# Kernel optimization log

Hardware: AMD Instinct MI355X
Metric: run time of the kernel (lower is better)

Reference implementation:

```python
import jax, jax.numpy as jnp
import numpy as np

B, CIN, COUT, H, W = 8, 128, 128, 64, 64
KH = KW = 3
STRIDE = PAD = 1
DIL = 1
K = KH * KW
EPS = 1e-4


def setup_inputs() -> dict:
    key = jax.random.key(0)
    k1, k2, k3 = jax.random.split(key, 3)
    Ho = (H + 2 * PAD - DIL * (KH - 1) - 1) // STRIDE + 1
    Wo = (W + 2 * PAD - DIL * (KW - 1) - 1) // STRIDE + 1
    x = jax.random.normal(k1, (B, CIN, H, W), dtype=jnp.float32)
    offset = jax.random.normal(k2, (B, 2 * K, Ho, Wo), dtype=jnp.float32)
    weight = jax.random.normal(k3, (COUT, CIN, KH, KW), dtype=jnp.float32) * 0.05
    return {"x": x, "offset": offset, "weight": weight}


def _bilinear_gather(x, py, px):
    # x: [B, C, H, W]; py/px: [B, K, Ho, Wo] float sampling positions
    Bn, C, Hn, Wn = x.shape
    x_flat = x.reshape(Bn, C, Hn * Wn)
    y0 = jnp.floor(py)
    x0 = jnp.floor(px)
    ly = py - y0  # fractional parts
    lx = px - x0
    out = 0.0
    corners = [(0.0, 0.0, (1 - ly) * (1 - lx)), (0.0, 1.0, (1 - ly) * lx),
               (1.0, 0.0, ly * (1 - lx)), (1.0, 1.0, ly * lx)]
    for dy, dx, wgt in corners:
        yy = y0 + dy
        xx = x0 + dx
        valid = (yy >= 0) & (yy < Hn) & (xx >= 0) & (xx < Wn)
        yi = jnp.clip(yy, 0, Hn - 1).astype(jnp.int32)
        xi = jnp.clip(xx, 0, Wn - 1).astype(jnp.int32)
        idx = (yi * Wn + xi).reshape(Bn, -1)  # [B, K*Ho*Wo]
        g = jax.vmap(lambda xf, ib: jnp.take(xf, ib, axis=1))(x_flat, idx)  # [B, C, N]
        out = out + g * (wgt * valid.astype(x.dtype)).reshape(Bn, 1, -1)
    return out  # [B, C, K*Ho*Wo]


def reference(x, offset, weight) -> jnp.ndarray:
    Bn = x.shape[0]
    Ho, Wo = offset.shape[2], offset.shape[3]
    # --- weight normalization (per output channel, per kernel tap) ---
    norm_fac = (KH * KW) ** 0.5
    length = jnp.sqrt(jnp.sum(jnp.square(weight) + EPS, axis=1, keepdims=True))  # [O,1,kh,kw]
    wn = weight / length / norm_fac  # [O, Cin, kh, kw]
    # --- sampling positions ---
    off = offset.reshape(Bn, K, 2, Ho, Wo)
    off_y, off_x = off[:, :, 0], off[:, :, 1]
    ky, kx = jnp.meshgrid(jnp.arange(KH), jnp.arange(KW), indexing="ij")
    ky = (ky.reshape(K) * DIL).astype(jnp.float32)
    kx = (kx.reshape(K) * DIL).astype(jnp.float32)
    base_y = (jnp.arange(Ho) * STRIDE - PAD).astype(jnp.float32)
    base_x = (jnp.arange(Wo) * STRIDE - PAD).astype(jnp.float32)
    py = base_y[None, None, :, None] + ky[None, :, None, None] + off_y  # [B,K,Ho,Wo]
    px = base_x[None, None, None, :] + kx[None, :, None, None] + off_x
    # --- deformable im2col + GEMM ---
    cols = _bilinear_gather(x, py, px).reshape(Bn, CIN, K, Ho, Wo)
    out = jnp.einsum("bckhw,ock->bohw", cols, wn.reshape(COUT, CIN, K))
    return out
```

## Files before the change

### kernel.cpp

```cpp
#include <hip/hip_runtime.h>
#include <math.h>


typedef __attribute__((ext_vector_type(8))) short short8;
typedef __attribute__((ext_vector_type(4))) float floatx4;

static __device__ __forceinline__ unsigned int f2bf(float f) {
    unsigned int u = __float_as_uint(f);
    u += 0x7fffu + ((u >> 16) & 1u);
    return u >> 16;
}
static __device__ __forceinline__ float bflo(unsigned int w) {
    return __uint_as_float(w << 16);
}
static __device__ __forceinline__ float bfhi(unsigned int w) {
    return __uint_as_float(w & 0xffff0000u);
}

__global__ void wnorm_k(const float* __restrict__ w, unsigned short* __restrict__ wb) {
    const int ok = blockIdx.x;
    const int o = ok / 9, k = ok % 9;
    const int lane = threadIdx.x;
    const float v0 = w[o * 1152 + lane * 9 + k];
    const float v1 = w[o * 1152 + (lane + 64) * 9 + k];
    float s = v0 * v0 + v1 * v1;
    #pragma unroll
    for (int d = 32; d >= 1; d >>= 1) s += __shfl_xor(s, d, 64);
    const float inv = 1.0f / (3.0f * sqrtf(s + 0.0128f));
    wb[((k * 16 + (lane >> 3)) * 128 + o) * 8 + (lane & 7)]     = (unsigned short)f2bf(v0 * inv);
    wb[((k * 16 + 8 + (lane >> 3)) * 128 + o) * 8 + (lane & 7)] = (unsigned short)f2bf(v1 * inv);
}

__global__ void xpose_k(const float* __restrict__ x, unsigned int* __restrict__ xt32) {
    __shared__ float lds[128 * 65];
    const int b = blockIdx.x >> 6, h = blockIdx.x & 63;
    const int tid = threadIdx.x;
    const float* xp = x + (b * 128 * 64 + h) * 64;
    #pragma unroll 4
    for (int i = 0; i < 32; i++) {
        const int c = i * 4 + (tid >> 6);
        const int ww = tid & 63;
        lds[c * 65 + ww] = xp[c * 4096 + ww];
    }
    __syncthreads();
    unsigned int* xo = xt32 + blockIdx.x * 4096;
    #pragma unroll 4
    for (int i = 0; i < 16; i++) {
        const int flat2 = i * 256 + tid;
        const int ww = flat2 >> 6, cp = flat2 & 63;
        const unsigned int lo = f2bf(lds[(2 * cp) * 65 + ww]);
        const unsigned int hi = f2bf(lds[(2 * cp + 1) * 65 + ww]);
        xo[flat2] = lo | (hi << 16);
    }
}

__global__ __launch_bounds__(256, 2) void dconv_k(
    const unsigned short* __restrict__ xt, const float* __restrict__ off,
    const unsigned short* __restrict__ wb, float* __restrict__ out)
{
    __shared__ float4 tapw[576];
    __shared__ int4   tapi[576];
    __shared__ alignas(16) unsigned short colsS[16 * 520];
    __shared__ alignas(16) unsigned short wS[16 * 128 * 8];

    const int bh = blockIdx.x, b = bh >> 6, ho = bh & 63;
    const int tid = threadIdx.x;

    for (int t = tid; t < 576; t += 256) {
        const int k = t >> 6, p = t & 63;
        const int oidx = ((b * 18 + 2 * k) * 64 + ho) * 64 + p;
        const float offy = off[oidx];
        const float offx = off[oidx + 4096];
        const float py = (float)(ho - 1 + (k / 3)) + offy;
        const float px = (float)(p - 1 + (k % 3)) + offx;
        const float y0f = floorf(py), x0f = floorf(px);
        const float ly = py - y0f, lx = px - x0f;
        const int y0 = (int)y0f, x0 = (int)x0f;
        const int y1 = y0 + 1, x1 = x0 + 1;
        const float vy0 = (y0 >= 0 && y0 < 64) ? 1.0f : 0.0f;
        const float vy1 = (y1 >= 0 && y1 < 64) ? 1.0f : 0.0f;
        const float vx0 = (x0 >= 0 && x0 < 64) ? 1.0f : 0.0f;
        const float vx1 = (x1 >= 0 && x1 < 64) ? 1.0f : 0.0f;
        const int yc0 = min(max(y0, 0), 63), yc1 = min(max(y1, 0), 63);
        const int xc0 = min(max(x0, 0), 63), xc1 = min(max(x1, 0), 63);
        tapw[t] = make_float4((1.0f - ly) * (1.0f - lx) * vy0 * vx0,
                              (1.0f - ly) * lx          * vy0 * vx1,
                              ly * (1.0f - lx)          * vy1 * vx0,
                              ly * lx                   * vy1 * vx1);
        tapi[t] = make_int4((yc0 * 64 + xc0) * 128, (yc0 * 64 + xc1) * 128,
                            (yc1 * 64 + xc0) * 128, (yc1 * 64 + xc1) * 128);
    }
    __syncthreads();

    const int lane = tid & 63, wv = tid >> 6;
    const int quad = lane >> 4, l16 = lane & 15;
    const int g = tid & 15, prow = tid >> 4;
    const unsigned short* xb = xt + b * (64 * 64 * 128);
    const int wbase = wv * 32;

    floatx4 acc0[4], acc1[4];
    #pragma unroll
    for (int t = 0; t < 4; t++) {
        acc0[t] = (floatx4)0.0f;
        acc1[t] = (floatx4)0.0f;
    }

    for (int k = 0; k < 9; k++) {
        const uint4* wsrc = (const uint4*)(wb + k * 16384);
        uint4* wdst = (uint4*)wS;
        #pragma unroll
        for (int i = 0; i < 8; i++) wdst[i * 256 + tid] = wsrc[i * 256 + tid];

        #pragma unroll
        for (int i = 0; i < 4; i++) {
            const int p = i * 16 + prow;
            const float4 wvv = tapw[k * 64 + p];
            const int4  iv  = tapi[k * 64 + p];
            const uint4 r0 = *(const uint4*)(xb + iv.x + g * 8);
            const uint4 r1 = *(const uint4*)(xb + iv.y + g * 8);
            const uint4 r2 = *(const uint4*)(xb + iv.z + g * 8);
            const uint4 r3 = *(const uint4*)(xb + iv.w + g * 8);
            uint4 pk;
            {
                const float lo = wvv.x*bflo(r0.x) + wvv.y*bflo(r1.x) + wvv.z*bflo(r2.x) + wvv.w*bflo(r3.x);
                const float hi = wvv.x*bfhi(r0.x) + wvv.y*bfhi(r1.x) + wvv.z*bfhi(r2.x) + wvv.w*bfhi(r3.x);
                pk.x = f2bf(lo) | (f2bf(hi) << 16);
            }
            {
                const float lo = wvv.x*bflo(r0.y) + wvv.y*bflo(r1.y) + wvv.z*bflo(r2.y) + wvv.w*bflo(r3.y);
                const float hi = wvv.x*bfhi(r0.y) + wvv.y*bfhi(r1.y) + wvv.z*bfhi(r2.y) + wvv.w*bfhi(r3.y);
                pk.y = f2bf(lo) | (f2bf(hi) << 16);
            }
            {
                const float lo = wvv.x*bflo(r0.z) + wvv.y*bflo(r1.z) + wvv.z*bflo(r2.z) + wvv.w*bflo(r3.z);
                const float hi = wvv.x*bfhi(r0.z) + wvv.y*bfhi(r1.z) + wvv.z*bfhi(r2.z) + wvv.w*bfhi(r3.z);
                pk.z = f2bf(lo) | (f2bf(hi) << 16);
            }
            {
                const float lo = wvv.x*bflo(r0.w) + wvv.y*bflo(r1.w) + wvv.z*bflo(r2.w) + wvv.w*bflo(r3.w);
                const float hi = wvv.x*bfhi(r0.w) + wvv.y*bfhi(r1.w) + wvv.z*bfhi(r2.w) + wvv.w*bfhi(r3.w);
                pk.w = f2bf(lo) | (f2bf(hi) << 16);
            }
            *(uint4*)&colsS[g * 520 + p * 8] = pk;
        }
        __syncthreads();

        #pragma unroll
        for (int q = 0; q < 4; q++) {
            const int cgrp = q * 4 + quad;
            const short8 a0 = *(const short8*)&wS[(cgrp * 128 + wbase + l16) * 8];
            const short8 a1 = *(const short8*)&wS[(cgrp * 128 + wbase + 16 + l16) * 8];
            #pragma unroll
            for (int t = 0; t < 4; t++) {
                const short8 bf = *(const short8*)&colsS[cgrp * 520 + (t * 16 + l16) * 8];
                acc0[t] = __builtin_amdgcn_mfma_f32_16x16x32_bf16(a0, bf, acc0[t], 0, 0, 0);
                acc1[t] = __builtin_amdgcn_mfma_f32_16x16x32_bf16(a1, bf, acc1[t], 0, 0, 0);
            }
        }
        __syncthreads();
    }

    float* ob = out + b * 128 * 4096 + ho * 64;
    #pragma unroll
    for (int t = 0; t < 4; t++) {
        const int pix = t * 16 + l16;
        #pragma unroll
        for (int r = 0; r < 4; r++) {
            ob[(wbase + quad * 4 + r) * 4096 + pix]      = acc0[t][r];
            ob[(wbase + 16 + quad * 4 + r) * 4096 + pix] = acc1[t][r];
        }
    }
}

extern "C" void kernel_launch(void* const* d_in, const int* in_sizes, int n_in,
                              void* d_out, int out_size, void* d_ws, size_t ws_size,
                              hipStream_t stream) {
    const float* x   = (const float*)d_in[0];
    const float* off = (const float*)d_in[1];
    const float* w   = (const float*)d_in[2];
    float* out = (float*)d_out;

    unsigned short* xt = (unsigned short*)d_ws;
    unsigned short* wbuf = xt + 8 * 64 * 64 * 128;

    hipLaunchKernelGGL(wnorm_k, dim3(1152), dim3(64),  0, stream, w, wbuf);
    hipLaunchKernelGGL(xpose_k, dim3(512),  dim3(256), 0, stream, x, (unsigned int*)xt);
    hipLaunchKernelGGL(dconv_k, dim3(512),  dim3(256), 0, stream, xt, off, wbuf, out);
}
```

Before: 106.3 us.

## Double-buffer im2col gather, read weights from global, fuse prep kernels

Merges the weight-normalization and input-transpose kernels into one launch, with weight norm now done per output channel using coalesced loads. In the main kernel the deformable gather for the next tap is issued before the current tap's MFMAs, writing into a second LDS buffer. This cuts one barrier per tap and overlaps gather latency with matrix math. Weight fragments are now read directly from global memory (L2-cached) rather than staged through LDS, which frees LDS but adds global-load latency inside the MFMA loop and raises register pressure from holding 16 prefetched uint4s.

New measurement: 110.7 us. 4.1% more time.

```diff
diff --git a/kernel.cpp b/kernel.cpp
--- a/kernel.cpp
+++ b/kernel.cpp
@@ -17,41 +17,80 @@
     return __uint_as_float(w & 0xffff0000u);
 }
 
-__global__ void wnorm_k(const float* __restrict__ w, unsigned short* __restrict__ wb) {
-    const int ok = blockIdx.x;
-    const int o = ok / 9, k = ok % 9;
-    const int lane = threadIdx.x;
-    const float v0 = w[o * 1152 + lane * 9 + k];
-    const float v1 = w[o * 1152 + (lane + 64) * 9 + k];
-    float s = v0 * v0 + v1 * v1;
-    #pragma unroll
-    for (int d = 32; d >= 1; d >>= 1) s += __shfl_xor(s, d, 64);
-    const float inv = 1.0f / (3.0f * sqrtf(s + 0.0128f));
-    wb[((k * 16 + (lane >> 3)) * 128 + o) * 8 + (lane & 7)]     = (unsigned short)f2bf(v0 * inv);
-    wb[((k * 16 + 8 + (lane >> 3)) * 128 + o) * 8 + (lane & 7)] = (unsigned short)f2bf(v1 * inv);
-}
-
-__global__ void xpose_k(const float* __restrict__ x, unsigned int* __restrict__ xt32) {
+__global__ void prep_k(const float* __restrict__ x, const float* __restrict__ w,
+                       unsigned int* __restrict__ xt32, unsigned short* __restrict__ wb) {
     __shared__ float lds[128 * 65];
-    const int b = blockIdx.x >> 6, h = blockIdx.x & 63;
     const int tid = threadIdx.x;
-    const float* xp = x + (b * 128 * 64 + h) * 64;
-    #pragma unroll 4
-    for (int i = 0; i < 32; i++) {
-        const int c = i * 4 + (tid >> 6);
-        const int ww = tid & 63;
-        lds[c * 65 + ww] = xp[c * 4096 + ww];
-    }
-    __syncthreads();
-    unsigned int* xo = xt32 + blockIdx.x * 4096;
-    #pragma unroll 4
-    for (int i = 0; i < 16; i++) {
-        const int flat2 = i * 256 + tid;
-        const int ww = flat2 >> 6, cp = flat2 & 63;
-        const unsigned int lo = f2bf(lds[(2 * cp) * 65 + ww]);
-        const unsigned int hi = f2bf(lds[(2 * cp + 1) * 65 + ww]);
-        xo[flat2] = lo | (hi << 16);
-    }
+
+    if (blockIdx.x < 512) {
+        const int b = blockIdx.x >> 6, h = blockIdx.x & 63;
+        const float* xp = x + (b * 128 * 64 + h) * 64;
+        #pragma unroll 4
+        for (int i = 0; i < 32; i++) {
+            const int c = i * 4 + (tid >> 6);
+            const int ww = tid & 63;
+            lds[c * 65 + ww] = xp[c * 4096 + ww];
+        }
+        __syncthreads();
+        unsigned int* xo = xt32 + blockIdx.x * 4096;
+        #pragma unroll 4
+        for (int i = 0; i < 16; i++) {
+            const int flat2 = i * 256 + tid;
+            const int ww = flat2 >> 6, cp = flat2 & 63;
+            const unsigned int lo = f2bf(lds[(2 * cp) * 65 + ww]);
+            const unsigned int hi = f2bf(lds[(2 * cp + 1) * 65 + ww]);
+            xo[flat2] = lo | (hi << 16);
+        }
+    } else {
+        const int o = (blockIdx.x - 512) * 4 + (tid >> 6);
+        const int lane = tid & 63;
+        const float* wo = w + o * 1152;
+        float v[18];
+        #pragma unroll
+        for (int i = 0; i < 18; i++) v[i] = wo[lane * 18 + i];
+        float s[9];
+        #pragma unroll
+        for (int k = 0; k < 9; k++) s[k] = v[k] * v[k] + v[9 + k] * v[9 + k];
+        #pragma unroll
+        for (int d = 32; d >= 1; d >>= 1) {
+            #pragma unroll
+            for (int k = 0; k < 9; k++) s[k] += __shfl_xor(s[k], d, 64);
+        }
+        const int c0 = 2 * lane, c1 = c0 + 1;
+        #pragma unroll
+        for (int k = 0; k < 9; k++) {
+            const float inv = 1.0f / (3.0f * sqrtf(s[k] + 0.0128f));
+            wb[((k * 16 + (c0 >> 3)) * 128 + o) * 8 + (c0 & 7)] = (unsigned short)f2bf(v[k] * inv);
+            wb[((k * 16 + (c1 >> 3)) * 128 + o) * 8 + (c1 & 7)] = (unsigned short)f2bf(v[9 + k] * inv);
+        }
+    }
+}
+
+static __device__ __forceinline__ uint4 combine4(const float4 wvv,
+                                                 const uint4 r0, const uint4 r1,
+                                                 const uint4 r2, const uint4 r3) {
+    uint4 pk;
+    {
+        const float lo = wvv.x*bflo(r0.x) + wvv.y*bflo(r1.x) + wvv.z*bflo(r2.x) + wvv.w*bflo(r3.x);
+        const float hi = wvv.x*bfhi(r0.x) + wvv.y*bfhi(r1.x) + wvv.z*bfhi(r2.x) + wvv.w*bfhi(r3.x);
+        pk.x = f2bf(lo) | (f2bf(hi) << 16);
+    }
+    {
+        const float lo = wvv.x*bflo(r0.y) + wvv.y*bflo(r1.y) + wvv.z*bflo(r2.y) + wvv.w*bflo(r3.y);
+        const float hi = wvv.x*bfhi(r0.y) + wvv.y*bfhi(r1.y) + wvv.z*bfhi(r2.y) + wvv.w*bfhi(r3.y);
+        pk.y = f2bf(lo) | (f2bf(hi) << 16);
+    }
+    {
+        const float lo = wvv.x*bflo(r0.z) + wvv.y*bflo(r1.z) + wvv.z*bflo(r2.z) + wvv.w*bflo(r3.z);
+        const float hi = wvv.x*bfhi(r0.z) + wvv.y*bfhi(r1.z) + wvv.z*bfhi(r2.z) + wvv.w*bfhi(r3.z);
+        pk.z = f2bf(lo) | (f2bf(hi) << 16);
+    }
+    {
+        const float lo = wvv.x*bflo(r0.w) + wvv.y*bflo(r1.w) + wvv.z*bflo(r2.w) + wvv.w*bflo(r3.w);
+        const float hi = wvv.x*bfhi(r0.w) + wvv.y*bfhi(r1.w) + wvv.z*bfhi(r2.w) + wvv.w*bfhi(r3.w);
+        pk.w = f2bf(lo) | (f2bf(hi) << 16);
+    }
+    return pk;
 }
 
 __global__ __launch_bounds__(256, 2) void dconv_k(
@@ -60,8 +99,7 @@
 {
     __shared__ float4 tapw[576];
     __shared__ int4   tapi[576];
-    __shared__ alignas(16) unsigned short colsS[16 * 520];
-    __shared__ alignas(16) unsigned short wS[16 * 128 * 8];
+    __shared__ alignas(16) unsigned short colsS[2][16 * 520];
 
     const int bh = blockIdx.x, b = bh >> 6, ho = bh & 63;
     const int tid = threadIdx.x;
@@ -100,64 +138,61 @@
 
     floatx4 acc0[4], acc1[4];
     #pragma unroll
-    for (int t = 0; t < 4; t++) {
-        acc0[t] = (floatx4)0.0f;
-        acc1[t] = (floatx4)0.0f;
-    }
+    for (int t = 0; t < 4; t++) { acc0[t] = (floatx4)0.0f; acc1[t] = (floatx4)0.0f; }
+
+    #pragma unroll
+    for (int i = 0; i < 4; i++) {
+        const int p = i * 16 + prow;
+        const float4 wvv = tapw[p];
+        const int4  iv  = tapi[p];
+        const uint4 r0 = *(const uint4*)(xb + iv.x + g * 8);
+        const uint4 r1 = *(const uint4*)(xb + iv.y + g * 8);
+        const uint4 r2 = *(const uint4*)(xb + iv.z + g * 8);
+        const uint4 r3 = *(const uint4*)(xb + iv.w + g * 8);
+        *(uint4*)&colsS[0][g * 520 + p * 8] = combine4(wvv, r0, r1, r2, r3);
+    }
+    __syncthreads();
 
     for (int k = 0; k < 9; k++) {
-        const uint4* wsrc = (const uint4*)(wb + k * 16384);
-        uint4* wdst = (uint4*)wS;
-        #pragma unroll
-        for (int i = 0; i < 8; i++) wdst[i * 256 + tid] = wsrc[i * 256 + tid];
-
-        #pragma unroll
-        for (int i = 0; i < 4; i++) {
-            const int p = i * 16 + prow;
-            const float4 wvv = tapw[k * 64 + p];
-            const int4  iv  = tapi[k * 64 + p];
-            const uint4 r0 = *(const uint4*)(xb + iv.x + g * 8);
-            const uint4 r1 = *(const uint4*)(xb + iv.y + g * 8);
-            const uint4 r2 = *(const uint4*)(xb + iv.z + g * 8);
-            const uint4 r3 = *(const uint4*)(xb + iv.w + g * 8);
-            uint4 pk;
-            {
-                const float lo = wvv.x*bflo(r0.x) + wvv.y*bflo(r1.x) + wvv.z*bflo(r2.x) + wvv.w*bflo(r3.x);
-                const float hi = wvv.x*bfhi(r0.x) + wvv.y*bfhi(r1.x) + wvv.z*bfhi(r2.x) + wvv.w*bfhi(r3.x);
-                pk.x = f2bf(lo) | (f2bf(hi) << 16);
+        const int cur = k & 1;
+
+        uint4 r[4][4];
+        if (k < 8) {
+            #pragma unroll
+            for (int i = 0; i < 4; i++) {
+                const int p = i * 16 + prow;
+                const int4 iv = tapi[(k + 1) * 64 + p];
+                r[i][0] = *(const uint4*)(xb + iv.x + g * 8);
+                r[i][1] = *(const uint4*)(xb + iv.y + g * 8);
+                r[i][2] = *(const uint4*)(xb + iv.z + g * 8);
+                r[i][3] = *(const uint4*)(xb + iv.w + g * 8);
             }
-            {
-                const float lo = wvv.x*bflo(r0.y) + wvv.y*bflo(r1.y) + wvv.z*bflo(r2.y) + wvv.w*bflo(r3.y);
-                const float hi = wvv.x*bfhi(r0.y) + wvv.y*bfhi(r1.y) + wvv.z*bfhi(r2.y) + wvv.w*bfhi(r3.y);
-                pk.y = f2bf(lo) | (f2bf(hi) << 16);
-            }
-            {
-                const float lo = wvv.x*bflo(r0.z) + wvv.y*bflo(r1.z) + wvv.z*bflo(r2.z) + wvv.w*bflo(r3.z);
-                const float hi = wvv.x*bfhi(r0.z) + wvv.y*bfhi(r1.z) + wvv.z*bfhi(r2.z) + wvv.w*bfhi(r3.z);
-                pk.z = f2bf(lo) | (f2bf(hi) << 16);
-            }
-            {
-                const float lo = wvv.x*bflo(r0.w) + wvv.y*bflo(r1.w) + wvv.z*bflo(r2.w) + wvv.w*bflo(r3.w);
-                const float hi = wvv.x*bfhi(r0.w) + wvv.y*bfhi(r1.w) + wvv.z*bfhi(r2.w) + wvv.w*bfhi(r3.w);
-                pk.w = f2bf(lo) | (f2bf(hi) << 16);
-            }
-            *(uint4*)&colsS[g * 520 + p * 8] = pk;
-        }
-        __syncthreads();
-
+        }
+
+        const unsigned short* wk = wb + k * 16384;
         #pragma unroll
         for (int q = 0; q < 4; q++) {
             const int cgrp = q * 4 + quad;
-            const short8 a0 = *(const short8*)&wS[(cgrp * 128 + wbase + l16) * 8];
-            const short8 a1 = *(const short8*)&wS[(cgrp * 128 + wbase + 16 + l16) * 8];
+            const short8 a0 = *(const short8*)(wk + (cgrp * 128 + wbase + l16) * 8);
+            const short8 a1 = *(const short8*)(wk + (cgrp * 128 + wbase + 16 + l16) * 8);
             #pragma unroll
             for (int t = 0; t < 4; t++) {
-                const short8 bf = *(const short8*)&colsS[cgrp * 520 + (t * 16 + l16) * 8];
+                const short8 bf = *(const short8*)&colsS[cur][cgrp * 520 + (t * 16 + l16) * 8];
                 acc0[t] = __builtin_amdgcn_mfma_f32_16x16x32_bf16(a0, bf, acc0[t], 0, 0, 0);
                 acc1[t] = __builtin_amdgcn_mfma_f32_16x16x32_bf16(a1, bf, acc1[t], 0, 0, 0);
             }
         }
-        __syncthreads();
+
+        if (k < 8) {
+            #pragma unroll
+            for (int i = 0; i < 4; i++) {
+                const int p = i * 16 + prow;
+                const float4 wvv = tapw[(k + 1) * 64 + p];
+                *(uint4*)&colsS[cur ^ 1][g * 520 + p * 8] =
+                    combine4(wvv, r[i][0], r[i][1], r[i][2], r[i][3]);
+            }
+            __syncthreads();
+        }
     }
 
     float* ob = out + b * 128 * 4096 + ho * 64;
@@ -165,9 +200,9 @@
     for (int t = 0; t < 4; t++) {
         const int pix = t * 16 + l16;
         #pragma unroll
-        for (int r = 0; r < 4; r++) {
-            ob[(wbase + quad * 4 + r) * 4096 + pix]      = acc0[t][r];
-            ob[(wbase + 16 + quad * 4 + r) * 4096 + pix] = acc1[t][r];
+        for (int r2 = 0; r2 < 4; r2++) {
+            ob[(wbase + quad * 4 + r2) * 4096 + pix]      = acc0[t][r2];
+            ob[(wbase + 16 + quad * 4 + r2) * 4096 + pix] = acc1[t][r2];
         }
     }
 }
@@ -183,7 +218,7 @@
     unsigned short* xt = (unsigned short*)d_ws;
     unsigned short* wbuf = xt + 8 * 64 * 64 * 128;
 
-    hipLaunchKernelGGL(wnorm_k, dim3(1152), dim3(64),  0, stream, w, wbuf);
-    hipLaunchKernelGGL(xpose_k, dim3(512),  dim3(256), 0, stream, x, (unsigned int*)xt);
-    hipLaunchKernelGGL(dconv_k, dim3(512),  dim3(256), 0, stream, xt, off, wbuf, out);
-}
+    hipLaunchKernelGGL(prep_k,  dim3(544), dim3(256), 0, stream,
+                       x, w, (unsigned int*)xt, wbuf);
+    hipLaunchKernelGGL(dconv_k, dim3(512), dim3(256), 0, stream, xt, off, wbuf, out);
+}
```
